# Optimization experiments

Hardware: AMD Instinct MI355X
Metric: run time of the kernel (lower is better)

Reference implementation:

```python
import jax, jax.numpy as jnp
import numpy as np

D_MODEL = 2048
B, T, N = 4, 2048, 512


def setup_inputs() -> dict:
    key = jax.random.key(0)
    k1, k2, k3, k4, k5 = jax.random.split(key, 5)
    x = jax.random.normal(k1, (B, T, D_MODEL), dtype=jnp.float32)
    h_stack = jax.random.normal(k2, (B, N, D_MODEL), dtype=jnp.float32)
    m_stack = jax.random.normal(k3, (B, N, D_MODEL), dtype=jnp.float32)
    m_current = jax.random.normal(k4, (B, T, D_MODEL), dtype=jnp.float32)
    # block-causal visibility: position t can see cache entry j iff j <= t*N/T
    causal_mask = jnp.arange(N)[None, :] <= (jnp.arange(T)[:, None] * N // T)
    # learned projection, torch Linear stores weight as (out, in): u = x @ W.T
    W_u = jax.random.normal(k5, (D_MODEL, D_MODEL), dtype=jnp.float32) * (1.0 / np.sqrt(D_MODEL))
    return {"x": x, "h_stack": h_stack, "m_stack": m_stack,
            "m_current": m_current, "causal_mask": causal_mask, "W_u": W_u}


def reference(x, h_stack, m_stack, m_current, causal_mask, W_u):
    D = x.shape[-1]
    n = m_stack.shape[1]
    scale = 1.0 / jnp.sqrt(jnp.asarray(D, x.dtype))
    u = jnp.einsum('btd,ed->bte', x, W_u)                      # Linear(no bias): x @ W.T
    scores_cached = jnp.einsum('btd,bnd->btn', u, m_stack) * scale
    neg_inf = jnp.asarray(-jnp.inf, scores_cached.dtype)
    scores_cached = jnp.where(causal_mask[None, :, :], scores_cached, neg_inf)
    scores_current = jnp.sum(u * m_current, axis=-1, keepdims=True) * scale  # (B,T,1)
    all_scores = jnp.concatenate([scores_cached, scores_current], axis=-1)   # (B,T,N+1)
    attn_weights = jax.nn.softmax(all_scores, axis=-1)
    gates_cached = attn_weights[:, :, :n]
    gate_current = attn_weights[:, :, n:]
    h_retrieved = jnp.einsum('btn,bnd->btd', gates_cached, h_stack)
    return h_retrieved, gate_current, attn_weights
```

## Files before the change

### kernel.cpp

```cpp
#include <hip/hip_runtime.h>

#define D_MODEL 2048
#define B_SZ 4
#define T_SZ 2048
#define N_SZ 512

typedef __bf16 bf16x8 __attribute__((ext_vector_type(8)));
typedef float f32x4 __attribute__((ext_vector_type(4)));
typedef ushort u16x8 __attribute__((ext_vector_type(8)));

__device__ __forceinline__ ushort f2bf(float f) {
  unsigned u = __float_as_uint(f);
  unsigned r = (u + 0x7fffu + ((u >> 16) & 1u)) >> 16;
  return (ushort)r;
}
__device__ __forceinline__ float bflo(unsigned w) { return __uint_as_float(w << 16); }
__device__ __forceinline__ float bfhi(unsigned w) { return __uint_as_float(w & 0xffff0000u); }

__device__ __forceinline__ void async_ld16(const ushort* g, ushort* l) {
  __builtin_amdgcn_global_load_lds(
      (const __attribute__((address_space(1))) void*)g,
      (__attribute__((address_space(3))) void*)l, 16, 0, 0);
}

__global__ __launch_bounds__(256) void conv_all(const float* __restrict__ x,
                                                const float* __restrict__ W,
                                                const float* __restrict__ ms,
                                                ushort* __restrict__ x_bf,
                                                ushort* __restrict__ W_bf,
                                                ushort* __restrict__ ms_bf) {
  const int bid = blockIdx.x;
  const float* src;
  ushort* dst;
  long blk;
  if (bid < 8192) { src = x; dst = x_bf; blk = bid; }
  else if (bid < 10240) { src = W; dst = W_bf; blk = bid - 8192; }
  else { src = ms; dst = ms_bf; blk = bid - 10240; }
  const long i = (blk * 256 + threadIdx.x) * 8;
  float4 a = *(const float4*)(src + i);
  float4 b = *(const float4*)(src + i + 4);
  u16x8 o;
  o[0] = f2bf(a.x); o[1] = f2bf(a.y); o[2] = f2bf(a.z); o[3] = f2bf(a.w);
  o[4] = f2bf(b.x); o[5] = f2bf(b.y); o[6] = f2bf(b.z); o[7] = f2bf(b.w);
  *(u16x8*)(dst + i) = o;
}

__global__ __launch_bounds__(256) void transpose_conv(const float* __restrict__ src,
                                                      ushort* __restrict__ dst) {
  __shared__ ushort tile[32][33];
  const int b = blockIdx.z;
  const int n0 = blockIdx.x * 32, d0 = blockIdx.y * 32;
  const int tx = threadIdx.x, ty = threadIdx.y;
  const float* s = src + (long)b * N_SZ * D_MODEL;
  ushort* d = dst + (long)b * D_MODEL * N_SZ;
#pragma unroll
  for (int r = 0; r < 4; r++)
    tile[ty + r * 8][tx] = f2bf(s[(long)(n0 + ty + r * 8) * D_MODEL + d0 + tx]);
  __syncthreads();
#pragma unroll
  for (int r = 0; r < 4; r++)
    d[(long)(d0 + ty + r * 8) * N_SZ + n0 + tx] = tile[tx][ty + r * 8];
}

template <int TM, int MASKMODE, bool OUT_BF16>
__global__ __launch_bounds__(256) void gemm_bt(const ushort* __restrict__ A,
                                               const ushort* __restrict__ Bt,
                                               void* __restrict__ Cv, int N, int K,
                                               long sA, long sB, long sC, float scale) {
  constexpr int NA = TM / 16;
  constexpr int NCH = NA + 8;
  constexpr int NC = NCH / 4;
  constexpr int NI = TM / 32;
  __shared__ __align__(16) ushort sa[TM * 32];
  __shared__ __align__(16) ushort sb[128 * 32];
  const int bz = blockIdx.z;
  const int row0 = blockIdx.y * TM;
  const int col0 = blockIdx.x * 128;
  if (MASKMODE == 1 && col0 > ((row0 + TM - 1) >> 2)) return;
  int Kend = K;
  if (MASKMODE == 2) {
    int kl = ((row0 + TM - 1) >> 2) + 1;
    Kend = min(K, (kl + 31) & ~31);
  }
  const ushort* Ab = A + (long)bz * sA;
  const ushort* Bb = Bt + (long)bz * sB;

  const int tid = threadIdx.x;
  const int w = tid >> 6, lane = tid & 63;
  const int wr = w >> 1, wc = w & 1;
  const int quad = lane >> 4, l16 = lane & 15;

  f32x4 acc[NI][4];
#pragma unroll
  for (int i = 0; i < NI; i++)
#pragma unroll
    for (int j = 0; j < 4; j++) acc[i][j] = (f32x4){0.f, 0.f, 0.f, 0.f};

  const int lrow = lane >> 2;
  const int lcol = (lane & 3) * 8;
  const ushort* gsrc[NC];
  ushort* ldst[NC];
#pragma unroll
  for (int t = 0; t < NC; t++) {
    const int c = w * NC + t;
    if (c < NA) {
      ldst[t] = sa + c * 512;
      gsrc[t] = Ab + (long)(row0 + c * 16 + lrow) * K + lcol;
    } else {
      ldst[t] = sb + (c - NA) * 512;
      gsrc[t] = Bb + (long)(col0 + (c - NA) * 16 + lrow) * K + lcol;
    }
  }

  for (int k0 = 0; k0 < Kend; k0 += 32) {
#pragma unroll
    for (int t = 0; t < NC; t++) async_ld16(gsrc[t] + k0, ldst[t]);
    __syncthreads();
    bf16x8 af[NI], bfr[4];
#pragma unroll
    for (int i = 0; i < NI; i++)
      af[i] = *(const bf16x8*)(sa + (wr * (TM / 2) + i * 16 + l16) * 32 + quad * 8);
#pragma unroll
    for (int j = 0; j < 4; j++)
      bfr[j] = *(const bf16x8*)(sb + (wc * 64 + j * 16 + l16) * 32 + quad * 8);
#pragma unroll
    for (int i = 0; i < NI; i++)
#pragma unroll
      for (int j = 0; j < 4; j++)
        acc[i][j] = __builtin_amdgcn_mfma_f32_16x16x32_bf16(af[i], bfr[j], acc[i][j], 0, 0, 0);
    __syncthreads();
  }

#pragma unroll
  for (int i = 0; i < NI; i++) {
    const int rb = row0 + wr * (TM / 2) + i * 16 + quad * 4;
#pragma unroll
    for (int j = 0; j < 4; j++) {
      const int c = col0 + wc * 64 + j * 16 + l16;
#pragma unroll
      for (int r = 0; r < 4; r++) {
        float v = acc[i][j][r] * scale;
        long off = (long)bz * sC + (long)(rb + r) * N + c;
        if (OUT_BF16)
          ((ushort*)Cv)[off] = f2bf(v);
        else
          ((float*)Cv)[off] = v;
      }
    }
  }
}

template <int MASKMODE, bool OUT_BF16>
__global__ __launch_bounds__(512, 2) void gemm256(const ushort* __restrict__ A,
                                                  const ushort* __restrict__ Bt,
                                                  void* __restrict__ Cv, int N, int K,
                                                  long sA, long sB, long sC, float scale) {
  __shared__ __align__(16) ushort lds[2][2][256 * 64];
  const int bz = blockIdx.z;
  const int row0 = blockIdx.y * 256;
  const int col0 = blockIdx.x * 256;
  int Kend = K;
  if (MASKMODE == 2) {
    int kl = ((row0 + 255) >> 2) + 1;
    Kend = min(K, (kl + 63) & ~63);
  }
  const int NT = Kend >> 6;
  const ushort* Ab = A + (long)bz * sA;
  const ushort* Bb = Bt + (long)bz * sB;

  const int tid = threadIdx.x;
  const int w = tid >> 6, lane = tid & 63;
  const int wr = w >> 2, wc = w & 3;
  const int quad = lane >> 4, l16 = lane & 15;

  f32x4 acc[8][4];
#pragma unroll
  for (int i = 0; i < 8; i++)
#pragma unroll
    for (int j = 0; j < 4; j++) acc[i][j] = (f32x4){0.f, 0.f, 0.f, 0.f};

  const int lrow = lane >> 3;
  const int lcol = ((lane & 7) ^ lrow) << 3;
  const ushort* gA[4];
  const ushort* gB[4];
#pragma unroll
  for (int j = 0; j < 4; j++) {
    gA[j] = Ab + (long)(row0 + j * 64 + w * 8 + lrow) * K + lcol;
    gB[j] = Bb + (long)(col0 + j * 64 + w * 8 + lrow) * K + lcol;
  }

#define GPHASE(MQ, NQ)                                                                   \
  do {                                                                                   \
    bf16x8 af[4][2], bv[2][2];                                                           \
    _Pragma("unroll") for (int m = 0; m < 4; m++) _Pragma("unroll")                      \
        for (int ks = 0; ks < 2; ks++) {                                                 \
      const int row = wr * 128 + MQ * 64 + m * 16 + l16;                                 \
      af[m][ks] = *(const bf16x8*)&lds[cbuf][0]                                          \
          [row * 64 + ((ks * 32 + quad * 8) ^ ((l16 & 7) << 3))];                        \
    }                                                                                    \
    _Pragma("unroll") for (int n = 0; n < 2; n++) _Pragma("unroll")                      \
        for (int ks = 0; ks < 2; ks++) {                                                 \
      const int row = wc * 64 + NQ * 32 + n * 16 + l16;                                  \
      bv[n][ks] = *(const bf16x8*)&lds[cbuf][1]                                          \
          [row * 64 + ((ks * 32 + quad * 8) ^ ((l16 & 7) << 3))];                        \
    }                                                                                    \
    __builtin_amdgcn_s_barrier();                                                        \
    __builtin_amdgcn_s_setprio(1);                                                       \
    _Pragma("unroll") for (int m = 0; m < 4; m++) _Pragma("unroll")                      \
        for (int n = 0; n < 2; n++) _Pragma("unroll")                                    \
            for (int ks = 0; ks < 2; ks++)                                               \
      acc[MQ * 4 + m][NQ * 2 + n] = __builtin_amdgcn_mfma_f32_16x16x32_bf16(             \
          af[m][ks], bv[n][ks], acc[MQ * 4 + m][NQ * 2 + n], 0, 0, 0);                   \
    __builtin_amdgcn_s_setprio(0);                                                       \
    __builtin_amdgcn_s_barrier();                                                        \
  } while (0)

#pragma unroll
  for (int j = 0; j < 4; j++) {
    async_ld16(gA[j], &lds[0][0][j * 4096 + w * 512]);
    async_ld16(gB[j], &lds[0][1][j * 4096 + w * 512]);
  }

  for (int t = 0; t < NT; ++t) {
    const int cbuf = t & 1;
    const int kn = (t + 1) << 6;
    if (t + 1 < NT) {
      async_ld16(gA[0] + kn, &lds[cbuf ^ 1][0][0 * 4096 + w * 512]);
      async_ld16(gB[0] + kn, &lds[cbuf ^ 1][1][0 * 4096 + w * 512]);
      asm volatile("s_waitcnt vmcnt(2)" ::: "memory");
    } else {
      asm volatile("s_waitcnt vmcnt(0)" ::: "memory");
    }
    __builtin_amdgcn_s_barrier();
    GPHASE(0, 0);
    if (t + 1 < NT) {
      async_ld16(gA[1] + kn, &lds[cbuf ^ 1][0][1 * 4096 + w * 512]);
      async_ld16(gB[1] + kn, &lds[cbuf ^ 1][1][1 * 4096 + w * 512]);
    }
    GPHASE(0, 1);
    if (t + 1 < NT) {
      async_ld16(gA[2] + kn, &lds[cbuf ^ 1][0][2 * 4096 + w * 512]);
      async_ld16(gB[2] + kn, &lds[cbuf ^ 1][1][2 * 4096 + w * 512]);
    }
    GPHASE(1, 0);
    if (t + 1 < NT) {
      async_ld16(gA[3] + kn, &lds[cbuf ^ 1][0][3 * 4096 + w * 512]);
      async_ld16(gB[3] + kn, &lds[cbuf ^ 1][1][3 * 4096 + w * 512]);
    }
    GPHASE(1, 1);
  }
#undef GPHASE

#pragma unroll
  for (int i = 0; i < 8; i++) {
    const int rb = row0 + wr * 128 + (i >> 2) * 64 + (i & 3) * 16 + quad * 4;
#pragma unroll
    for (int j = 0; j < 4; j++) {
      const int cc = col0 + wc * 64 + (j >> 1) * 32 + (j & 1) * 16 + l16;
#pragma unroll
      for (int r = 0; r < 4; r++) {
        float v = acc[i][j][r] * scale;
        long off = (long)bz * sC + (long)(rb + r) * N + cc;
        if (OUT_BF16)
          ((ushort*)Cv)[off] = f2bf(v);
        else
          ((float*)Cv)[off] = v;
      }
    }
  }
}

__global__ __launch_bounds__(256) void softmax_gate(const ushort* __restrict__ u_bf,
                                                    const float* __restrict__ m_cur,
                                                    const float* __restrict__ scores,
                                                    float* __restrict__ out_gc,
                                                    float* __restrict__ out_attn,
                                                    ushort* __restrict__ gates_bf) {
  const int wv = threadIdx.x >> 6, lane = threadIdx.x & 63;
  const int bt = blockIdx.x * 4 + wv;
  const int t = bt & (T_SZ - 1);
  const ushort* urow = u_bf + (long)bt * D_MODEL;
  const float* mrow = m_cur + (long)bt * D_MODEL;

  float part = 0.f;
#pragma unroll
  for (int c = 0; c < 4; c++) {
    uint4 uv = *(const uint4*)(urow + c * 512 + lane * 8);
    float4 m0 = *(const float4*)(mrow + c * 512 + lane * 8);
    float4 m1 = *(const float4*)(mrow + c * 512 + lane * 8 + 4);
    part += bflo(uv.x) * m0.x + bfhi(uv.x) * m0.y + bflo(uv.y) * m0.z + bfhi(uv.y) * m0.w +
            bflo(uv.z) * m1.x + bfhi(uv.z) * m1.y + bflo(uv.w) * m1.z + bfhi(uv.w) * m1.w;
  }
#pragma unroll
  for (int m = 32; m; m >>= 1) part += __shfl_xor(part, m, 64);
  const float curs = part * 0.022097086912079608f;

  const int nmax = t >> 2;
  const float* srow = scores + (long)bt * N_SZ;
  float sc[8];
  float lmax = curs;
#pragma unroll
  for (int k = 0; k < 8; k++) {
    const int n = k * 64 + lane;
    sc[k] = srow[n];
    if (n <= nmax) lmax = fmaxf(lmax, sc[k]);
  }
#pragma unroll
  for (int m = 32; m; m >>= 1) lmax = fmaxf(lmax, __shfl_xor(lmax, m, 64));

  float lsum = (lane == 0) ? __expf(curs - lmax) : 0.f;
#pragma unroll
  for (int k = 0; k < 8; k++) {
    const int n = k * 64 + lane;
    sc[k] = (n <= nmax) ? __expf(sc[k] - lmax) : 0.f;
    lsum += sc[k];
  }
#pragma unroll
  for (int m = 32; m; m >>= 1) lsum += __shfl_xor(lsum, m, 64);
  const float inv = 1.f / lsum;

  float* arow = out_attn + (long)bt * (N_SZ + 1);
  ushort* grow = gates_bf + (long)bt * N_SZ;
#pragma unroll
  for (int k = 0; k < 8; k++) {
    const int n = k * 64 + lane;
    const float wgt = sc[k] * inv;
    arow[n] = wgt;
    grow[n] = f2bf(wgt);
  }
  if (lane == 0) {
    const float g = __expf(curs - lmax) * inv;
    arow[N_SZ] = g;
    out_gc[bt] = g;
  }
}

extern "C" void kernel_launch(void* const* d_in, const int* in_sizes, int n_in,
                              void* d_out, int out_size, void* d_ws, size_t ws_size,
                              hipStream_t stream) {
  const float* x = (const float*)d_in[0];
  const float* h_stack = (const float*)d_in[1];
  const float* m_stack = (const float*)d_in[2];
  const float* m_cur = (const float*)d_in[3];
  const float* W = (const float*)d_in[5];

  float* out = (float*)d_out;
  float* out_h = out;
  float* out_gc = out + (long)B_SZ * T_SZ * D_MODEL;
  float* out_attn = out_gc + B_SZ * T_SZ;

  char* ws = (char*)d_ws;
  ushort* x_bf = (ushort*)ws;
  ushort* u_bf = x_bf + 16777216;
  ushort* W_bf = u_bf + 16777216;
  ushort* ms_bf = W_bf + 4194304;
  ushort* gates = ms_bf + 4194304;
  ushort* hsT = gates + 4194304;
  float* scores = (float*)(hsT + 4194304);

  conv_all<<<12288, 256, 0, stream>>>(x, W, m_stack, x_bf, W_bf, ms_bf);
  transpose_conv<<<dim3(N_SZ / 32, D_MODEL / 32, B_SZ), dim3(32, 8), 0, stream>>>(h_stack, hsT);

  gemm256<0, true><<<dim3(D_MODEL / 256, (B_SZ * T_SZ) / 256, 1), 512, 0, stream>>>(
      x_bf, W_bf, u_bf, D_MODEL, D_MODEL, 0, 0, 0, 1.0f);

  gemm_bt<64, 1, false><<<dim3(N_SZ / 128, T_SZ / 64, B_SZ), 256, 0, stream>>>(
      u_bf, ms_bf, scores, N_SZ, D_MODEL, (long)T_SZ * D_MODEL, (long)N_SZ * D_MODEL,
      (long)T_SZ * N_SZ, 0.022097086912079608f);

  softmax_gate<<<(B_SZ * T_SZ) / 4, 256, 0, stream>>>(u_bf, m_cur, scores, out_gc, out_attn,
                                                      gates);

  gemm256<2, false><<<dim3(D_MODEL / 256, T_SZ / 256, B_SZ), 512, 0, stream>>>(
      gates, hsT, out_h, D_MODEL, N_SZ, (long)T_SZ * N_SZ, (long)D_MODEL * N_SZ,
      (long)T_SZ * D_MODEL, 1.0f);
}
```

Before: 363.7 us.

## Reorder GEMM prefetch stages to match quadrant consumption order with finer vmcnt waits

Restructures the double-buffered GEMM main loop so each global-to-LDS prefetch chunk matches the A/B sub-tiles consumed by the next phase (A rows 0/128, B rows 0/128, B rows 32/160, A rows 64/192). Each phase now waits only on the chunks it needs through staggered vmcnt counts, and sched_barrier keeps the compiler from moving those waits. The goal is to start MFMA work on partially arrived tiles and hide global load latency better. The tighter vmcnt bookkeeping is fragile: a wrong count could read stale LDS data.

New measurement: 362.2 us. About the same (-0.4%).

```diff
diff --git a/kernel.cpp b/kernel.cpp
--- a/kernel.cpp
+++ b/kernel.cpp
@@ -181,75 +181,146 @@
 
   const int lrow = lane >> 3;
   const int lcol = ((lane & 7) ^ lrow) << 3;
-  const ushort* gA[4];
-  const ushort* gB[4];
-#pragma unroll
-  for (int j = 0; j < 4; j++) {
-    gA[j] = Ab + (long)(row0 + j * 64 + w * 8 + lrow) * K + lcol;
-    gB[j] = Bb + (long)(col0 + j * 64 + w * 8 + lrow) * K + lcol;
-  }
-
-#define GPHASE(MQ, NQ)                                                                   \
-  do {                                                                                   \
-    bf16x8 af[4][2], bv[2][2];                                                           \
-    _Pragma("unroll") for (int m = 0; m < 4; m++) _Pragma("unroll")                      \
-        for (int ks = 0; ks < 2; ks++) {                                                 \
-      const int row = wr * 128 + MQ * 64 + m * 16 + l16;                                 \
-      af[m][ks] = *(const bf16x8*)&lds[cbuf][0]                                          \
-          [row * 64 + ((ks * 32 + quad * 8) ^ ((l16 & 7) << 3))];                        \
-    }                                                                                    \
-    _Pragma("unroll") for (int n = 0; n < 2; n++) _Pragma("unroll")                      \
-        for (int ks = 0; ks < 2; ks++) {                                                 \
-      const int row = wc * 64 + NQ * 32 + n * 16 + l16;                                  \
-      bv[n][ks] = *(const bf16x8*)&lds[cbuf][1]                                          \
-          [row * 64 + ((ks * 32 + quad * 8) ^ ((l16 & 7) << 3))];                        \
-    }                                                                                    \
-    __builtin_amdgcn_s_barrier();                                                        \
-    __builtin_amdgcn_s_setprio(1);                                                       \
-    _Pragma("unroll") for (int m = 0; m < 4; m++) _Pragma("unroll")                      \
-        for (int n = 0; n < 2; n++) _Pragma("unroll")                                    \
-            for (int ks = 0; ks < 2; ks++)                                               \
-      acc[MQ * 4 + m][NQ * 2 + n] = __builtin_amdgcn_mfma_f32_16x16x32_bf16(             \
-          af[m][ks], bv[n][ks], acc[MQ * 4 + m][NQ * 2 + n], 0, 0, 0);                   \
-    __builtin_amdgcn_s_setprio(0);                                                       \
-    __builtin_amdgcn_s_barrier();                                                        \
+  const int bwA = w * 8;
+  const int bwB = ((w >> 2) << 6) + ((w & 3) << 3);
+
+  const ushort* a00 = Ab + (long)(row0 + bwA + lrow) * K + lcol;
+  const ushort* a01 = a00 + (long)128 * K;
+  const ushort* a30 = a00 + (long)64 * K;
+  const ushort* a31 = a00 + (long)192 * K;
+  const ushort* b10 = Bb + (long)(col0 + bwB + lrow) * K + lcol;
+  const ushort* b11 = b10 + (long)128 * K;
+  const ushort* b20 = b10 + (long)32 * K;
+  const ushort* b21 = b10 + (long)160 * K;
+
+  const uint dA00 = (uint)(bwA)*64, dA01 = (uint)(bwA + 128) * 64;
+  const uint dA30 = (uint)(bwA + 64) * 64, dA31 = (uint)(bwA + 192) * 64;
+  const uint dB10 = (uint)(bwB)*64, dB11 = (uint)(bwB + 128) * 64;
+  const uint dB20 = (uint)(bwB + 32) * 64, dB21 = (uint)(bwB + 160) * 64;
+
+#define STG_R0(nb, kk)                                    \
+  do {                                                    \
+    async_ld16(a00 + (kk), &lds[nb][0][dA00]);            \
+    async_ld16(a01 + (kk), &lds[nb][0][dA01]);            \
   } while (0)
-
-#pragma unroll
-  for (int j = 0; j < 4; j++) {
-    async_ld16(gA[j], &lds[0][0][j * 4096 + w * 512]);
-    async_ld16(gB[j], &lds[0][1][j * 4096 + w * 512]);
-  }
+#define STG_R1(nb, kk)                                    \
+  do {                                                    \
+    async_ld16(b10 + (kk), &lds[nb][1][dB10]);            \
+    async_ld16(b11 + (kk), &lds[nb][1][dB11]);            \
+  } while (0)
+#define STG_R2(nb, kk)                                    \
+  do {                                                    \
+    async_ld16(b20 + (kk), &lds[nb][1][dB20]);            \
+    async_ld16(b21 + (kk), &lds[nb][1][dB21]);            \
+  } while (0)
+#define STG_R3(nb, kk)                                    \
+  do {                                                    \
+    async_ld16(a30 + (kk), &lds[nb][0][dA30]);            \
+    async_ld16(a31 + (kk), &lds[nb][0][dA31]);            \
+  } while (0)
+
+#define LDA_(MQ)                                                            \
+  _Pragma("unroll") for (int m = 0; m < 4; m++) _Pragma("unroll")           \
+  for (int ks = 0; ks < 2; ks++) {                                          \
+    const int row = wr * 128 + (MQ)*64 + m * 16 + l16;                      \
+    af[m][ks] = *(const bf16x8*)&lds[cbuf][0]                               \
+        [row * 64 + ((ks * 32 + quad * 8) ^ ((l16 & 7) << 3))];             \
+  }
+#define LDB_(NQ)                                                            \
+  _Pragma("unroll") for (int n = 0; n < 2; n++) _Pragma("unroll")           \
+  for (int ks = 0; ks < 2; ks++) {                                          \
+    const int row = wc * 64 + (NQ)*32 + n * 16 + l16;                       \
+    bv[n][ks] = *(const bf16x8*)&lds[cbuf][1]                               \
+        [row * 64 + ((ks * 32 + quad * 8) ^ ((l16 & 7) << 3))];             \
+  }
+#define MM_(MQ, NQ)                                                         \
+  __builtin_amdgcn_s_setprio(1);                                            \
+  _Pragma("unroll") for (int m = 0; m < 4; m++) _Pragma("unroll")           \
+  for (int n = 0; n < 2; n++) _Pragma("unroll")                             \
+  for (int ks = 0; ks < 2; ks++)                                            \
+    acc[(MQ)*4 + m][(NQ)*2 + n] = __builtin_amdgcn_mfma_f32_16x16x32_bf16(  \
+        af[m][ks], bv[n][ks], acc[(MQ)*4 + m][(NQ)*2 + n], 0, 0, 0);        \
+  __builtin_amdgcn_s_setprio(0);
+#define VMC(n) asm volatile("s_waitcnt vmcnt(" #n ")" ::: "memory")
+#define SCB __builtin_amdgcn_sched_barrier(0)
+#define BAR __builtin_amdgcn_s_barrier()
+
+  STG_R0(0, 0);
+  STG_R1(0, 0);
+  STG_R2(0, 0);
+  STG_R3(0, 0);
+  VMC(4);
+  SCB;
+  BAR;
 
   for (int t = 0; t < NT; ++t) {
     const int cbuf = t & 1;
+    const int nb = cbuf ^ 1;
     const int kn = (t + 1) << 6;
-    if (t + 1 < NT) {
-      async_ld16(gA[0] + kn, &lds[cbuf ^ 1][0][0 * 4096 + w * 512]);
-      async_ld16(gB[0] + kn, &lds[cbuf ^ 1][1][0 * 4096 + w * 512]);
-      asm volatile("s_waitcnt vmcnt(2)" ::: "memory");
-    } else {
-      asm volatile("s_waitcnt vmcnt(0)" ::: "memory");
-    }
-    __builtin_amdgcn_s_barrier();
-    GPHASE(0, 0);
-    if (t + 1 < NT) {
-      async_ld16(gA[1] + kn, &lds[cbuf ^ 1][0][1 * 4096 + w * 512]);
-      async_ld16(gB[1] + kn, &lds[cbuf ^ 1][1][1 * 4096 + w * 512]);
-    }
-    GPHASE(0, 1);
-    if (t + 1 < NT) {
-      async_ld16(gA[2] + kn, &lds[cbuf ^ 1][0][2 * 4096 + w * 512]);
-      async_ld16(gB[2] + kn, &lds[cbuf ^ 1][1][2 * 4096 + w * 512]);
-    }
-    GPHASE(1, 0);
-    if (t + 1 < NT) {
-      async_ld16(gA[3] + kn, &lds[cbuf ^ 1][0][3 * 4096 + w * 512]);
-      async_ld16(gB[3] + kn, &lds[cbuf ^ 1][1][3 * 4096 + w * 512]);
-    }
-    GPHASE(1, 1);
-  }
-#undef GPHASE
+    const bool more = (t + 1 < NT);
+    {
+      bf16x8 af[4][2], bv[2][2];
+      LDA_(0)
+      LDB_(0)
+      if (more) {
+        STG_R0(nb, kn);
+        STG_R1(nb, kn);
+        VMC(6);
+      } else {
+        VMC(2);
+      }
+      SCB;
+      BAR;
+      MM_(0, 0)
+      BAR;
+    }
+    {
+      bf16x8 af[4][2], bv[2][2];
+      LDA_(0)
+      LDB_(1)
+      if (more) {
+        STG_R2(nb, kn);
+        VMC(6);
+      } else {
+        VMC(0);
+      }
+      SCB;
+      BAR;
+      MM_(0, 1)
+      BAR;
+    }
+    {
+      bf16x8 af[4][2], bv[2][2];
+      LDA_(1)
+      LDB_(0)
+      if (more) STG_R3(nb, kn);
+      BAR;
+      MM_(1, 0)
+      BAR;
+    }
+    {
+      bf16x8 af[4][2], bv[2][2];
+      LDA_(1)
+      LDB_(1)
+      if (more) {
+        VMC(4);
+        SCB;
+      }
+      BAR;
+      MM_(1, 1)
+      BAR;
+    }
+  }
+#undef STG_R0
+#undef STG_R1
+#undef STG_R2
+#undef STG_R3
+#undef LDA_
+#undef LDB_
+#undef MM_
+#undef VMC
+#undef SCB
+#undef BAR
 
 #pragma unroll
   for (int i = 0; i < 8; i++) {
```
